# Kernel tuning notes

Hardware: AMD Instinct MI355X
Metric: run time of the kernel (lower is better)

The kernel has to match this reference:

```python
import jax, jax.numpy as jnp
import numpy as np
from jax import lax

B, T, H = 16, 4096, 512

def setup_inputs() -> dict:
    key = jax.random.key(0)
    ks = jax.random.split(key, 10)
    return {
        "query": jax.random.normal(ks[0], (B, 1, H), dtype=jnp.float32),
        "value": jax.random.normal(ks[1], (B, T, H), dtype=jnp.float32),
        "last_attn": jax.random.uniform(ks[2], (B, T), dtype=jnp.float32),
        "conv_w": jax.random.normal(ks[3], (H, 1, 3), dtype=jnp.float32) * 0.05,
        "conv_b": jax.random.normal(ks[4], (H,), dtype=jnp.float32) * 0.05,
        "Wq": jax.random.normal(ks[5], (H, H), dtype=jnp.float32) * (1.0 / np.sqrt(H)),
        "Wv": jax.random.normal(ks[6], (H, H), dtype=jnp.float32) * (1.0 / np.sqrt(H)),
        "bias": jax.random.uniform(ks[7], (H,), minval=-0.1, maxval=0.1, dtype=jnp.float32),
        "w_score": jax.random.normal(ks[8], (1, H), dtype=jnp.float32) * (1.0 / np.sqrt(H)),
        "b_score": jax.random.normal(ks[9], (1,), dtype=jnp.float32) * 0.05,
    }

def reference(query, value, last_attn, conv_w, conv_b, Wq, Wv, bias, w_score, b_score):
    # conv1d over last_attn: (B,1,T) -> (B,H,T), kernel 3, pad 1
    conv = lax.conv_general_dilated(
        last_attn[:, None, :], conv_w, window_strides=(1,), padding="SAME",
        dimension_numbers=("NCH", "OIH", "NCH"))
    conv_attn = conv.transpose(0, 2, 1) + conv_b           # (B,T,H)
    q = jnp.einsum("bqh,oh->bqo", query, Wq)               # (B,1,H), Linear w/o bias: x @ W.T
    v = jnp.einsum("bth,oh->bto", value, Wv)               # (B,T,H)
    e = jnp.tanh(q + v + conv_attn + bias)                 # (B,T,H) broadcast over q_len=1
    score = jnp.einsum("bth,h->bt", e, w_score[0]) + b_score[0]  # (B,T)
    # smoothing=True: sigmoid + L1 normalize
    s = jax.nn.sigmoid(score)
    attn = s / jnp.sum(s, axis=-1, keepdims=True)          # (B,T)
    context = jnp.einsum("bt,bth->bh", attn, value)        # (B,H)
    out = jnp.concatenate([context, query[:, 0, :]], axis=1)  # (B,2H)
    return out, attn
```

## Files before the change

kernel.cpp:

```cpp
#include <hip/hip_runtime.h>
#include <hip/hip_bf16.h>
#include <cstddef>

#define BB 16
#define TT 4096
#define HH 512

typedef _Float16 half8 __attribute__((ext_vector_type(8)));
typedef float f32x4 __attribute__((ext_vector_type(4)));

__global__ void prep_kernel(const float* __restrict__ query,
                            const float* __restrict__ conv_b,
                            const float* __restrict__ Wq,
                            const float* __restrict__ Wv,
                            const float* __restrict__ bias,
                            _Float16* __restrict__ Bpack,
                            float* __restrict__ qb,
                            float* __restrict__ ssum,
                            float* __restrict__ ctx) {
    int blk = blockIdx.x;
    int tid = threadIdx.x;
    if (blk < 128) {
        int tn = blk >> 2, kq = blk & 3;
        int kb = kq * 4 + (tid >> 6);
        int lane = tid & 63;
        int n = tn * 16 + (lane & 15);
        int k = kb * 32 + ((lane >> 4) << 3);
        const float4* src = (const float4*)(Wv + (size_t)n * HH + k);
        float4 v0 = src[0], v1 = src[1];
        half8 h = { (_Float16)v0.x, (_Float16)v0.y, (_Float16)v0.z, (_Float16)v0.w,
                    (_Float16)v1.x, (_Float16)v1.y, (_Float16)v1.z, (_Float16)v1.w };
        *(half8*)(Bpack + ((size_t)(kb * 32 + tn) * 64 + lane) * 8) = h;
    } else if (blk < 192) {
        int q = blk - 128;
        int b = q >> 2, oq = q & 3;
        __shared__ float qrow[HH];
        for (int i = tid; i < HH; i += 256) qrow[i] = query[b * HH + i];
        __syncthreads();
        int wave = tid >> 6, lane = tid & 63;
        float4 q1 = *(const float4*)(qrow + lane * 8);
        float4 q2 = *(const float4*)(qrow + lane * 8 + 4);
        for (int i = wave; i < 128; i += 4) {
            int o = oq * 128 + i;
            const float4* w = (const float4*)(Wq + (size_t)o * HH);
            float4 a = w[lane * 2], c = w[lane * 2 + 1];
            float acc = a.x * q1.x + a.y * q1.y + a.z * q1.z + a.w * q1.w
                      + c.x * q2.x + c.y * q2.y + c.z * q2.z + c.w * q2.w;
            #pragma unroll
            for (int off = 1; off < 64; off <<= 1) acc += __shfl_xor(acc, off, 64);
            if (lane == 0) qb[b * HH + o] = acc + bias[o] + conv_b[o];
        }
    } else {
        for (int i = tid; i < BB; i += 256) ssum[i] = 0.f;
        for (int i = tid; i < BB * HH; i += 256) ctx[i] = 0.f;
    }
}

__global__ __launch_bounds__(512, 4) void gemm_fused_kernel(
        const float* __restrict__ value,
        const float* __restrict__ last_attn,
        const float* __restrict__ conv_w,
        const float* __restrict__ w_score,
        const float* __restrict__ b_score,
        const _Float16* __restrict__ Bpack,
        const float* __restrict__ qb,
        float* __restrict__ sbuf,
        float* __restrict__ ssum,
        float* __restrict__ ctx) {
    __shared__ _Float16 As[64 * 512];
    __shared__ float sred[64][4];
    __shared__ float s_lds[64];

    int tid = threadIdx.x;
    int blk = blockIdx.x;
    int b = blk >> 6;
    int t0 = (blk & 63) << 5;
    t0 <<= 1;

    int lane = tid & 63;
    int w = tid >> 6, msub = w & 1, ng = w >> 1;
    int quad = lane >> 4, lm = lane & 15;

    {
        int st = tid >> 3, cc = tid & 7;
        const float4* pA = (const float4*)(value + ((size_t)(b * TT + t0 + st)) * HH) + cc * 2;
        #pragma unroll
        for (int u = 0; u < 8; ++u) {
            float4 v0 = pA[u * 16], v1 = pA[u * 16 + 1];
            int cph = (cc + u * 8) ^ (st & 7);
            half8 h = { (_Float16)v0.x, (_Float16)v0.y, (_Float16)v0.z, (_Float16)v0.w,
                        (_Float16)v1.x, (_Float16)v1.y, (_Float16)v1.z, (_Float16)v1.w };
            *(half8*)(As + st * 512 + cph * 8) = h;
        }
    }

    float rs[2][4];
    #pragma unroll
    for (int mt = 0; mt < 2; ++mt)
        #pragma unroll
        for (int j = 0; j < 4; ++j) rs[mt][j] = 0.f;

    __syncthreads();

    #pragma unroll 1
    for (int p = 0; p < 2; ++p) {
        f32x4 acc[2][4];
        #pragma unroll
        for (int mt = 0; mt < 2; ++mt)
            #pragma unroll
            for (int nt = 0; nt < 4; ++nt) { f32x4 z = {0.f,0.f,0.f,0.f}; acc[mt][nt] = z; }

        const _Float16* bp = Bpack + (size_t)(p * 16 + ng * 4) * 512 + lane * 8;
        half8 breg[2][4];
        #pragma unroll
        for (int nt = 0; nt < 4; ++nt)
            breg[0][nt] = *(const half8*)(bp + nt * 512);
        bp += 16384;

        #pragma unroll 2
        for (int kb = 0; kb < 16; ++kb) {
            int cb = kb & 1;
            if (kb < 15) {
                #pragma unroll
                for (int nt = 0; nt < 4; ++nt)
                    breg[cb ^ 1][nt] = *(const half8*)(bp + nt * 512);
                bp += 16384;
            }
            #pragma unroll
            for (int mt = 0; mt < 2; ++mt) {
                int tr = msub * 32 + mt * 16 + lm;
                int cph = ((kb << 2) + quad) ^ (tr & 7);
                half8 a = *(const half8*)(As + tr * 512 + cph * 8);
                #pragma unroll
                for (int nt = 0; nt < 4; ++nt)
                    acc[mt][nt] = __builtin_amdgcn_mfma_f32_16x16x32_f16(a, breg[cb][nt], acc[mt][nt], 0, 0, 0);
            }
        }

        #pragma unroll
        for (int nt = 0; nt < 4; ++nt) {
            int o = p * 256 + ng * 64 + nt * 16 + lm;
            float qv = qb[b * HH + o];
            float c0 = conv_w[o * 3 + 0];
            float c1 = conv_w[o * 3 + 1];
            float c2 = conv_w[o * 3 + 2];
            float wv = w_score[o];
            #pragma unroll
            for (int mt = 0; mt < 2; ++mt) {
                #pragma unroll
                for (int j = 0; j < 4; ++j) {
                    int tg = t0 + msub * 32 + mt * 16 + quad * 4 + j;
                    const float* la = last_attn + b * TT + tg;
                    float lam = (tg > 0) ? la[-1] : 0.f;
                    float la0 = la[0];
                    float lap = (tg < TT - 1) ? la[1] : 0.f;
                    float act = acc[mt][nt][j] + qv + c0 * lam + c1 * la0 + c2 * lap;
                    act = fminf(15.f, fmaxf(-15.f, act));
                    float e2 = __expf(2.f * act);
                    rs[mt][j] += ((e2 - 1.f) / (e2 + 1.f)) * wv;
                }
            }
        }
    }

    #pragma unroll
    for (int mt = 0; mt < 2; ++mt)
        #pragma unroll
        for (int j = 0; j < 4; ++j) {
            float v = rs[mt][j];
            #pragma unroll
            for (int off = 1; off < 16; off <<= 1) v += __shfl_xor(v, off, 64);
            if (lm == 0) {
                if (ng == 0) sred[msub * 32 + mt * 16 + quad * 4 + j][0] = v;
            }
        }
    __syncthreads();
    #pragma unroll
    for (int mt = 0; mt < 2; ++mt)
        #pragma unroll
        for (int j = 0; j < 4; ++j) {
            float v = rs[mt][j];
            #pragma unroll
            for (int off = 1; off < 16; off <<= 1) v += __shfl_xor(v, off, 64);
            if (lm == 0 && ng != 0)
                atomicAdd(&sred[msub * 32 + mt * 16 + quad * 4 + j][0], v);
        }
    __syncthreads();

    if (tid < 64) {
        float sc = b_score[0] + sred[tid][0];
        float s = 1.f / (1.f + __expf(-sc));
        s_lds[tid] = s;
        sbuf[b * TT + t0 + tid] = s;
        float tot = s;
        #pragma unroll
        for (int off = 1; off < 64; off <<= 1) tot += __shfl_xor(tot, off, 64);
        if (tid == 0) atomicAdd(&ssum[b], tot);
    }
    __syncthreads();

    {
        int h = tid;
        int cl = h >> 3, j = h & 7;
        float a = 0.f;
        #pragma unroll 8
        for (int t2 = 0; t2 < 64; ++t2) {
            int cph = cl ^ (t2 & 7);
            a += s_lds[t2] * (float)As[t2 * 512 + cph * 8 + j];
        }
        atomicAdd(&ctx[b * HH + h], a);
    }
}

__global__ void finalize_kernel(const float* __restrict__ query,
                                const float* __restrict__ ctx,
                                const float* __restrict__ sbuf,
                                const float* __restrict__ ssum,
                                float* __restrict__ out) {
    int idx = blockIdx.x * 256 + threadIdx.x;
    if (idx < BB * 2 * HH) {
        int b = idx >> 10, c = idx & 1023;
        float v;
        if (c < HH) v = ctx[b * HH + c] / ssum[b];
        else        v = query[b * HH + (c - HH)];
        out[idx] = v;
    } else {
        int j = idx - BB * 2 * HH;
        int b = j >> 12, t = j & 4095;
        out[idx] = sbuf[b * TT + t] / ssum[b];
    }
}

extern "C" void kernel_launch(void* const* d_in, const int* in_sizes, int n_in,
                              void* d_out, int out_size, void* d_ws, size_t ws_size,
                              hipStream_t stream) {
    const float* query     = (const float*)d_in[0];
    const float* value     = (const float*)d_in[1];
    const float* last_attn = (const float*)d_in[2];
    const float* conv_w    = (const float*)d_in[3];
    const float* conv_b    = (const float*)d_in[4];
    const float* Wq        = (const float*)d_in[5];
    const float* Wv        = (const float*)d_in[6];
    const float* bias      = (const float*)d_in[7];
    const float* w_score   = (const float*)d_in[8];
    const float* b_score   = (const float*)d_in[9];

    char* ws = (char*)d_ws;
    _Float16* Bpack = (_Float16*)ws;
    float* qb     = (float*)(ws + 524288);
    float* sbuf   = (float*)(ws + 557056);
    float* ssum   = (float*)(ws + 819200);
    float* ctx    = (float*)(ws + 819264);
    float* out    = (float*)d_out;

    prep_kernel<<<193, 256, 0, stream>>>(query, conv_b, Wq, Wv, bias, Bpack, qb, ssum, ctx);
    gemm_fused_kernel<<<1024, 512, 0, stream>>>(value, last_attn, conv_w, w_score,
                                                b_score, Bpack, qb, sbuf, ssum, ctx);
    finalize_kernel<<<320, 256, 0, stream>>>(query, ctx, sbuf, ssum, out);
}
```

Before: 279.6 us.

## Give each wave all 64 rows over one N-slice and drop LDS atomic reduction

Changes the warp decomposition so each of the 8 waves computes all 64 rows for its own 64 output columns in one pass, instead of two passes over 32-row halves. This removes the outer p loop and reloads B fragments once per wave. The cross-wave score reduction now writes per-wave partials to an 8-wide shared array and sums them in a single pass, replacing the second shuffle round and the LDS atomics. Tanh and sigmoid divisions become hardware reciprocals. The accumulators double to 64 floats per thread, which raises register pressure under launch_bounds(512,4) and may cause spills.

Measured after the change: 265.9 us. 1.05x faster.

```diff
diff --git a/kernel.cpp b/kernel.cpp
--- a/kernel.cpp
+++ b/kernel.cpp
@@ -8,6 +8,8 @@
 
 typedef _Float16 half8 __attribute__((ext_vector_type(8)));
 typedef float f32x4 __attribute__((ext_vector_type(4)));
+
+__device__ __forceinline__ float fast_rcp(float x) { return __builtin_amdgcn_rcpf(x); }
 
 __global__ void prep_kernel(const float* __restrict__ query,
                             const float* __restrict__ conv_b,
@@ -68,17 +70,15 @@
         float* __restrict__ ssum,
         float* __restrict__ ctx) {
     __shared__ _Float16 As[64 * 512];
-    __shared__ float sred[64][4];
+    __shared__ float sred[64][8];
     __shared__ float s_lds[64];
 
     int tid = threadIdx.x;
     int blk = blockIdx.x;
     int b = blk >> 6;
-    int t0 = (blk & 63) << 5;
-    t0 <<= 1;
-
-    int lane = tid & 63;
-    int w = tid >> 6, msub = w & 1, ng = w >> 1;
+    int t0 = (blk & 63) << 6;
+
+    int lane = tid & 63, ng = tid >> 6;
     int quad = lane >> 4, lm = lane & 15;
 
     {
@@ -94,102 +94,90 @@
         }
     }
 
-    float rs[2][4];
-    #pragma unroll
-    for (int mt = 0; mt < 2; ++mt)
-        #pragma unroll
-        for (int j = 0; j < 4; ++j) rs[mt][j] = 0.f;
+    f32x4 acc[4][4];
+    #pragma unroll
+    for (int mt = 0; mt < 4; ++mt)
+        #pragma unroll
+        for (int nt = 0; nt < 4; ++nt) { f32x4 z = {0.f,0.f,0.f,0.f}; acc[mt][nt] = z; }
+
+    const _Float16* bp = Bpack + (size_t)(ng * 4) * 512 + lane * 8;
+    half8 breg[2][4];
+    #pragma unroll
+    for (int nt = 0; nt < 4; ++nt)
+        breg[0][nt] = *(const half8*)(bp + nt * 512);
+    bp += 16384;
 
     __syncthreads();
 
-    #pragma unroll 1
-    for (int p = 0; p < 2; ++p) {
-        f32x4 acc[2][4];
-        #pragma unroll
-        for (int mt = 0; mt < 2; ++mt)
-            #pragma unroll
-            for (int nt = 0; nt < 4; ++nt) { f32x4 z = {0.f,0.f,0.f,0.f}; acc[mt][nt] = z; }
-
-        const _Float16* bp = Bpack + (size_t)(p * 16 + ng * 4) * 512 + lane * 8;
-        half8 breg[2][4];
-        #pragma unroll
-        for (int nt = 0; nt < 4; ++nt)
-            breg[0][nt] = *(const half8*)(bp + nt * 512);
-        bp += 16384;
-
-        #pragma unroll 2
-        for (int kb = 0; kb < 16; ++kb) {
-            int cb = kb & 1;
-            if (kb < 15) {
-                #pragma unroll
-                for (int nt = 0; nt < 4; ++nt)
-                    breg[cb ^ 1][nt] = *(const half8*)(bp + nt * 512);
-                bp += 16384;
+    #pragma unroll 2
+    for (int kb = 0; kb < 16; ++kb) {
+        int cb = kb & 1;
+        if (kb < 15) {
+            #pragma unroll
+            for (int nt = 0; nt < 4; ++nt)
+                breg[cb ^ 1][nt] = *(const half8*)(bp + nt * 512);
+            bp += 16384;
+        }
+        #pragma unroll
+        for (int mt = 0; mt < 4; ++mt) {
+            int tr = mt * 16 + lm;
+            int cph = ((kb << 2) + quad) ^ (tr & 7);
+            half8 a = *(const half8*)(As + tr * 512 + cph * 8);
+            #pragma unroll
+            for (int nt = 0; nt < 4; ++nt)
+                acc[mt][nt] = __builtin_amdgcn_mfma_f32_16x16x32_f16(a, breg[cb][nt], acc[mt][nt], 0, 0, 0);
+        }
+    }
+
+    float qvv[4], c0v[4], c1v[4], c2v[4], wvv[4];
+    #pragma unroll
+    for (int nt = 0; nt < 4; ++nt) {
+        int o = ng * 64 + nt * 16 + lm;
+        qvv[nt] = qb[b * HH + o];
+        c0v[nt] = conv_w[o * 3 + 0];
+        c1v[nt] = conv_w[o * 3 + 1];
+        c2v[nt] = conv_w[o * 3 + 2];
+        wvv[nt] = w_score[o];
+    }
+    float rs[4][4];
+    #pragma unroll
+    for (int mt = 0; mt < 4; ++mt) {
+        #pragma unroll
+        for (int j = 0; j < 4; ++j) {
+            int tg = t0 + mt * 16 + quad * 4 + j;
+            const float* la = last_attn + b * TT + tg;
+            float lam = (tg > 0) ? la[-1] : 0.f;
+            float la0 = la[0];
+            float lap = (tg < TT - 1) ? la[1] : 0.f;
+            float r = 0.f;
+            #pragma unroll
+            for (int nt = 0; nt < 4; ++nt) {
+                float act = acc[mt][nt][j] + qvv[nt]
+                          + c0v[nt] * lam + c1v[nt] * la0 + c2v[nt] * lap;
+                act = fminf(15.f, fmaxf(-15.f, act));
+                float e2 = __expf(2.f * act);
+                r += (1.f - 2.f * fast_rcp(e2 + 1.f)) * wvv[nt];
             }
-            #pragma unroll
-            for (int mt = 0; mt < 2; ++mt) {
-                int tr = msub * 32 + mt * 16 + lm;
-                int cph = ((kb << 2) + quad) ^ (tr & 7);
-                half8 a = *(const half8*)(As + tr * 512 + cph * 8);
-                #pragma unroll
-                for (int nt = 0; nt < 4; ++nt)
-                    acc[mt][nt] = __builtin_amdgcn_mfma_f32_16x16x32_f16(a, breg[cb][nt], acc[mt][nt], 0, 0, 0);
-            }
-        }
-
-        #pragma unroll
-        for (int nt = 0; nt < 4; ++nt) {
-            int o = p * 256 + ng * 64 + nt * 16 + lm;
-            float qv = qb[b * HH + o];
-            float c0 = conv_w[o * 3 + 0];
-            float c1 = conv_w[o * 3 + 1];
-            float c2 = conv_w[o * 3 + 2];
-            float wv = w_score[o];
-            #pragma unroll
-            for (int mt = 0; mt < 2; ++mt) {
-                #pragma unroll
-                for (int j = 0; j < 4; ++j) {
-                    int tg = t0 + msub * 32 + mt * 16 + quad * 4 + j;
-                    const float* la = last_attn + b * TT + tg;
-                    float lam = (tg > 0) ? la[-1] : 0.f;
-                    float la0 = la[0];
-                    float lap = (tg < TT - 1) ? la[1] : 0.f;
-                    float act = acc[mt][nt][j] + qv + c0 * lam + c1 * la0 + c2 * lap;
-                    act = fminf(15.f, fmaxf(-15.f, act));
-                    float e2 = __expf(2.f * act);
-                    rs[mt][j] += ((e2 - 1.f) / (e2 + 1.f)) * wv;
-                }
-            }
-        }
-    }
-
-    #pragma unroll
-    for (int mt = 0; mt < 2; ++mt)
+            rs[mt][j] = r;
+        }
+    }
+
+    #pragma unroll
+    for (int mt = 0; mt < 4; ++mt)
         #pragma unroll
         for (int j = 0; j < 4; ++j) {
             float v = rs[mt][j];
             #pragma unroll
             for (int off = 1; off < 16; off <<= 1) v += __shfl_xor(v, off, 64);
-            if (lm == 0) {
-                if (ng == 0) sred[msub * 32 + mt * 16 + quad * 4 + j][0] = v;
-            }
+            if (lm == 0) sred[mt * 16 + quad * 4 + j][ng] = v;
         }
     __syncthreads();
-    #pragma unroll
-    for (int mt = 0; mt < 2; ++mt)
-        #pragma unroll
-        for (int j = 0; j < 4; ++j) {
-            float v = rs[mt][j];
-            #pragma unroll
-            for (int off = 1; off < 16; off <<= 1) v += __shfl_xor(v, off, 64);
-            if (lm == 0 && ng != 0)
-                atomicAdd(&sred[msub * 32 + mt * 16 + quad * 4 + j][0], v);
-        }
-    __syncthreads();
 
     if (tid < 64) {
-        float sc = b_score[0] + sred[tid][0];
-        float s = 1.f / (1.f + __expf(-sc));
+        float sc = b_score[0];
+        #pragma unroll
+        for (int k = 0; k < 8; ++k) sc += sred[tid][k];
+        float s = fast_rcp(1.f + __expf(-sc));
         s_lds[tid] = s;
         sbuf[b * TT + t0 + tid] = s;
         float tot = s;
```
